# Performance work log

Hardware: AMD Instinct MI355X
Metric: run time of the kernel (lower is better)

Reference implementation:

```python
import jax, jax.numpy as jnp
import numpy as np

N_QUBITS = 10
Q_DEPTH = 6
MAX_LAYERS = 15
DIM = 2 ** N_QUBITS


def _apply_1q(s, U, w):
    # s: (B, 2^n) real statevector (circuit uses only H/RY/CNOT, all real).
    # Wire 0 is the most-significant bit (PennyLane convention).
    a, b = 2 ** w, 2 ** (N_QUBITS - 1 - w)
    s = s.reshape(-1, a, 2, b)
    if U.ndim == 2:  # gate shared across batch
        s = jnp.einsum('ij,Bajb->Baib', U, s)
    else:            # per-sample gate, U: (B,2,2)
        s = jnp.einsum('Bij,Bajb->Baib', U, s)
    return s.reshape(-1, DIM)


def _apply_cnot(s, c, t):
    # CNOT, control c < target t
    s = s.reshape(-1, 2 ** c, 2, 2 ** (t - c - 1), 2, 2 ** (N_QUBITS - 1 - t))
    s = jnp.stack([s[:, :, 0], jnp.flip(s[:, :, 1], axis=3)], axis=2)
    return s.reshape(-1, DIM)


def _ry(theta):
    # RY(theta) = [[cos t/2, -sin t/2], [sin t/2, cos t/2]]; theta scalar or (B,)
    c, si = jnp.cos(theta / 2.0), jnp.sin(theta / 2.0)
    return jnp.stack([jnp.stack([c, -si], -1), jnp.stack([si, c], -1)], -2)


def _quantum_net(q_in, q_params):
    # q_in: (B, n_qubits) rotation angles; q_params: (max_layers*n_qubits,)
    B = q_in.shape[0]
    qw = q_params.reshape(MAX_LAYERS, N_QUBITS)
    s = jnp.zeros((B, DIM), q_in.dtype).at[:, 0].set(1.0)  # |0...0>
    H = jnp.array([[1.0, 1.0], [1.0, -1.0]], q_in.dtype) / jnp.sqrt(jnp.asarray(2.0, q_in.dtype))
    for w in range(N_QUBITS):
        s = _apply_1q(s, H, w)
    for w in range(N_QUBITS):
        s = _apply_1q(s, _ry(q_in[:, w]), w)
    for k in range(Q_DEPTH):
        for i in range(0, N_QUBITS - 1, 2):
            s = _apply_cnot(s, i, i + 1)
        for i in range(1, N_QUBITS - 1, 2):
            s = _apply_cnot(s, i, i + 1)
        for w in range(N_QUBITS):
            s = _apply_1q(s, _ry(qw[k + 1, w]), w)
    probs = s * s
    # <Z_w> = P(bit_w = 0) - P(bit_w = 1)
    z = []
    for w in range(N_QUBITS):
        p = probs.reshape(-1, 2 ** w, 2, 2 ** (N_QUBITS - 1 - w)).sum(axis=(1, 3))
        z.append(p[:, 0] - p[:, 1])
    return jnp.stack(z, axis=1)  # (B, n_qubits)


def setup_inputs() -> dict:
    key = jax.random.key(0)
    ks = jax.random.split(key, 6)
    B, F, NQ, NC = 8192, 512, N_QUBITS, 2
    q_delta = 0.01
    return {
        'input_features': jax.random.normal(ks[0], (B, F), jnp.float32),
        'W_pre': jax.random.normal(ks[1], (NQ, F), jnp.float32) / np.sqrt(F),
        'b_pre': jnp.zeros((NQ,), jnp.float32),
        'q_params': q_delta * jax.random.normal(ks[2], (MAX_LAYERS * NQ,), jnp.float32),
        'W_post': jax.random.normal(ks[3], (NC, NQ), jnp.float32) / np.sqrt(NQ),
        'b_post': jnp.zeros((NC,), jnp.float32),
    }


def reference(input_features, W_pre, b_pre, q_params, W_post, b_post):
    pre_out = input_features @ W_pre.T + b_pre          # (B, n_qubits)
    q_in = jnp.tanh(pre_out) * (np.pi / 2.0)            # scale to [-pi/2, pi/2]
    q_out = _quantum_net(q_in, q_params)                # (B, n_qubits) PauliZ expvals
    return q_out @ W_post.T + b_post                    # (B, n_classes)
```

## Files before the change

### kernel.cpp

```cpp
#include <hip/hip_runtime.h>
#include <math.h>


#define NQ   10
#define NREG 16
#define DIM  1024

typedef _Float16 f16;
typedef _Float16 f16x8 __attribute__((ext_vector_type(8)));
typedef float    f32x4 __attribute__((ext_vector_type(4)));

template<int BB>
__device__ __forceinline__ void ry_lane(float (&s)[NREG], int lane, float c, float si) {
    float sgn = ((lane >> BB) & 1) ? si : -si;
    #pragma unroll
    for (int r = 0; r < NREG; ++r) {
        float o = __shfl_xor(s[r], 1 << BB);
        s[r] = fmaf(sgn, o, c * s[r]);
    }
}
template<int P>
__device__ __forceinline__ void ry_reg(float (&s)[NREG], float c, float si) {
    const int m = 1 << P;
    #pragma unroll
    for (int r = 0; r < NREG; ++r) {
        if ((r & m) == 0) {
            float a = s[r], b = s[r + m];
            s[r]     = fmaf(c, a, -si * b);
            s[r + m] = fmaf(si, a,  c * b);
        }
    }
}
__device__ __forceinline__ void cnot_5_6(float (&s)[NREG], int lane) {
    bool sel = (lane & 1) != 0;
    #pragma unroll
    for (int r = 0; r < 8; ++r) {
        float a = s[r], b = s[r + 8];
        s[r]     = sel ? b : a;
        s[r + 8] = sel ? a : b;
    }
}
template<int PC, int PT>
__device__ __forceinline__ void cnot_reg(float (&s)[NREG]) {
    #pragma unroll
    for (int r = 0; r < NREG; ++r) {
        if (((r >> PC) & 1) && !((r >> PT) & 1)) {
            float t = s[r];
            s[r] = s[r ^ (1 << PT)];
            s[r ^ (1 << PT)] = t;
        }
    }
}
__device__ __forceinline__ void perm_even(float (&s)[NREG], int lane) {
    int src = lane ^ (((((lane >> 5) & 1) << 4)) | ((((lane >> 3) & 1) << 2)) | (((lane >> 1) & 1)));
    #pragma unroll
    for (int r = 0; r < NREG; ++r) s[r] = __shfl(s[r], src);
}
__device__ __forceinline__ void perm_odd(float (&s)[NREG], int lane) {
    int src = lane ^ (((((lane >> 4) & 1) << 3)) | ((((lane >> 2) & 1) << 1)));
    #pragma unroll
    for (int r = 0; r < NREG; ++r) s[r] = __shfl(s[r], src);
}

#define APPLY_RY_ALL(CARR, SARR, BASE)                                        \
    { float c_, s_;                                                           \
      c_=__shfl(CARR,(BASE)+0); s_=__shfl(SARR,(BASE)+0); ry_lane<5>(s,lane,c_,s_); \
      c_=__shfl(CARR,(BASE)+1); s_=__shfl(SARR,(BASE)+1); ry_lane<4>(s,lane,c_,s_); \
      c_=__shfl(CARR,(BASE)+2); s_=__shfl(SARR,(BASE)+2); ry_lane<3>(s,lane,c_,s_); \
      c_=__shfl(CARR,(BASE)+3); s_=__shfl(SARR,(BASE)+3); ry_lane<2>(s,lane,c_,s_); \
      c_=__shfl(CARR,(BASE)+4); s_=__shfl(SARR,(BASE)+4); ry_lane<1>(s,lane,c_,s_); \
      c_=__shfl(CARR,(BASE)+5); s_=__shfl(SARR,(BASE)+5); ry_lane<0>(s,lane,c_,s_); \
      c_=__shfl(CARR,(BASE)+6); s_=__shfl(SARR,(BASE)+6); ry_reg<3>(s,c_,s_);       \
      c_=__shfl(CARR,(BASE)+7); s_=__shfl(SARR,(BASE)+7); ry_reg<2>(s,c_,s_);       \
      c_=__shfl(CARR,(BASE)+8); s_=__shfl(SARR,(BASE)+8); ry_reg<1>(s,c_,s_);       \
      c_=__shfl(CARR,(BASE)+9); s_=__shfl(SARR,(BASE)+9); ry_reg<0>(s,c_,s_); }

__device__ __forceinline__ void async16(const void* g, void* l) {
    __builtin_amdgcn_global_load_lds(
        (const __attribute__((address_space(1))) void*)g,
        (__attribute__((address_space(3))) void*)l, 16, 0, 0);
}

__global__ __launch_bounds__(256) void ka_prepare(
    const float* __restrict__ X, const float* __restrict__ Wpre,
    const float* __restrict__ bpre, const float* __restrict__ qp,
    f16* __restrict__ psi0, f16* __restrict__ Arm, float* __restrict__ z, int B)
{
    const int tid = threadIdx.x, lane = tid & 63, wv = tid >> 6;

    {
        int idx = blockIdx.x * 256 + tid;
        if (idx < 8192 * NQ) z[idx] = 0.0f;
    }

    for (int it = 0; it < 4; ++it) {
        int sample = blockIdx.x * 16 + wv * 4 + it;
        if (sample >= B) break;
        const float* xrow = X + (size_t)sample * 512;
        float4 x0 = ((const float4*)xrow)[lane];
        float4 x1 = ((const float4*)xrow)[64 + lane];
        float acc[NQ];
        #pragma unroll
        for (int q = 0; q < NQ; ++q) {
            const float* wr = Wpre + q * 512;
            float4 w0 = ((const float4*)wr)[lane];
            float4 w1 = ((const float4*)wr)[64 + lane];
            float a = x0.x * w0.x;
            a = fmaf(x0.y, w0.y, a); a = fmaf(x0.z, w0.z, a); a = fmaf(x0.w, w0.w, a);
            a = fmaf(x1.x, w1.x, a); a = fmaf(x1.y, w1.y, a);
            a = fmaf(x1.z, w1.z, a); a = fmaf(x1.w, w1.w, a);
            acc[q] = a;
        }
        #pragma unroll
        for (int q = 0; q < NQ; ++q) {
            float v = acc[q];
            #pragma unroll
            for (int d = 32; d >= 1; d >>= 1) v += __shfl_xor(v, d);
            acc[q] = v;
        }
        float pre = acc[0];
        #pragma unroll
        for (int q = 1; q < NQ; ++q) pre = (lane == q) ? acc[q] : pre;
        float c45 = 0.0f, s45 = 0.0f;
        if (lane < NQ) {
            float th = tanhf(pre + bpre[lane]) * 1.5707963267948966f;
            sincosf(0.5f * th + 0.7853981633974483f, &s45, &c45);
        }
        float lv = 1.0f;
        #pragma unroll
        for (int w = 0; w < 6; ++w) {
            float f0 = __shfl(c45, w), f1 = __shfl(s45, w);
            lv *= ((lane >> (5 - w)) & 1) ? f1 : f0;
        }
        float c6 = __shfl(c45, 6), s6 = __shfl(s45, 6);
        float c7 = __shfl(c45, 7), s7 = __shfl(s45, 7);
        float c8 = __shfl(c45, 8), s8 = __shfl(s45, 8);
        float c9 = __shfl(c45, 9), s9 = __shfl(s45, 9);
        float g01[4] = {c6 * c7, c6 * s7, s6 * c7, s6 * s7};
        float g23[4] = {c8 * c9, c8 * s9, s8 * c9, s8 * s9};
        union { f16 h[16]; float4 v[2]; } u;
        #pragma unroll
        for (int r = 0; r < NREG; ++r)
            u.h[r] = (f16)(lv * g01[r >> 2] * g23[r & 3]);
        float4* dst = (float4*)((char*)psi0 + (size_t)sample * 2048 + lane * 32);
        dst[0] = u.v[0];
        dst[1] = u.v[1];
    }

    if (wv < 2) {
        int row = blockIdx.x * 2 + wv;
        if (row < DIM) {
            float cw = 1.0f, swn = 0.0f;
            if (lane < 60) {
                float s_, c_;
                sincosf(0.5f * qp[10 + lane], &s_, &c_);
                cw = c_; swn = -s_;
            }
            float s[NREG];
            int srcLane = row >> 4, srcReg = row & 15;
            #pragma unroll
            for (int r = 0; r < NREG; ++r)
                s[r] = (lane == srcLane && r == srcReg) ? 1.0f : 0.0f;
            for (int kk = 6; kk >= 1; --kk) {
                APPLY_RY_ALL(cw, swn, (kk - 1) * 10);
                perm_odd(s, lane);
                cnot_5_6(s, lane);
                cnot_reg<2, 1>(s);
                perm_even(s, lane);
                cnot_reg<3, 2>(s);
                cnot_reg<1, 0>(s);
            }
            union { f16 h[16]; float4 v[2]; } u;
            #pragma unroll
            for (int r = 0; r < NREG; ++r) u.h[r] = (f16)s[r];
            float4* dst = (float4*)((char*)Arm + (size_t)row * 2048 + lane * 32);
            dst[0] = u.v[0];
            dst[1] = u.v[1];
        }
    }
}

__global__ __launch_bounds__(256, 4) void kb_gemm_measure(
    const f16* __restrict__ psi0, const f16* __restrict__ Arm,
    float* __restrict__ z)
{
    __shared__ __align__(16) char smem[24576];
    const int tid = threadIdx.x, lane = tid & 63, wv = tid >> 6;

    const int mB = blockIdx.x & 127, nB = blockIdx.x >> 7;
    const size_t tM = (size_t)mB * 64, tN = (size_t)nB * 128;
    f16* As = (f16*)smem;
    f16* Bs = (f16*)(smem + 8192);
    const int wm = (wv >> 1) * 32, wn = (wv & 1) * 64;

    f32x4 acc[2][4] = {};

    const f16* ga[2]; int ldsoA[2];
    #pragma unroll
    for (int p = 0; p < 2; ++p) {
        int slot = p * 256 + tid;
        int row = slot >> 3, gp = slot & 7, g = gp ^ (row & 7);
        ga[p] = psi0 + (tM + row) * 1024 + g * 8;
        ldsoA[p] = slot * 16;
    }
    const f16* gb[4]; int ldsoB[4];
    #pragma unroll
    for (int p = 0; p < 4; ++p) {
        int slot = p * 256 + tid;
        int row = slot >> 3, gp = slot & 7, g = gp ^ (row & 7);
        gb[p] = Arm + (tN + row) * 1024 + g * 8;
        ldsoB[p] = slot * 16;
    }

    for (int kt = 0; kt < 1024; kt += 64) {
        __syncthreads();
        #pragma unroll
        for (int p = 0; p < 2; ++p) async16(ga[p] + kt, (char*)As + ldsoA[p]);
        #pragma unroll
        for (int p = 0; p < 4; ++p) async16(gb[p] + kt, (char*)Bs + ldsoB[p]);
        __syncthreads();
        #pragma unroll
        for (int ks = 0; ks < 2; ++ks) {
            f16x8 af[2], bf[4];
            const int gpb = ks * 4 + (lane >> 4);
            const int gpx = gpb ^ (lane & 7);
            #pragma unroll
            for (int i = 0; i < 2; ++i) {
                int rowA = wm + i * 16 + (lane & 15);
                af[i] = *(const f16x8*)(As + rowA * 64 + gpx * 8);
            }
            #pragma unroll
            for (int j = 0; j < 4; ++j) {
                int rowB = wn + j * 16 + (lane & 15);
                bf[j] = *(const f16x8*)(Bs + rowB * 64 + gpx * 8);
            }
            #pragma unroll
            for (int i = 0; i < 2; ++i)
                #pragma unroll
                for (int j = 0; j < 4; ++j)
                    acc[i][j] = __builtin_amdgcn_mfma_f32_16x16x32_f16(af[i], bf[j], acc[i][j], 0, 0, 0);
        }
    }

    __syncthreads();
    float* zb = (float*)smem + (wn ? 640 : 0);
    const float sg0 = (nB & 4) ? -1.0f : 1.0f;
    const float sg1 = (nB & 2) ? -1.0f : 1.0f;
    const float sg2 = (nB & 1) ? -1.0f : 1.0f;
    const float sg3 = wn ? -1.0f : 1.0f;

    #pragma unroll
    for (int i = 0; i < 2; ++i) {
        #pragma unroll
        for (int t = 0; t < 4; ++t) {
            float p0 = acc[i][0][t] * acc[i][0][t];
            float p1 = acc[i][1][t] * acc[i][1][t];
            float p2 = acc[i][2][t] * acc[i][2][t];
            float p3 = acc[i][3][t] * acc[i][3][t];
            float t0  = (p0 + p1) + (p2 + p3);
            float tw5 = (p0 - p1) + (p2 - p3);
            float tw4 = (p0 + p1) - (p2 + p3);
            float s1 = __shfl_xor(t0, 1);
            float Av = t0 + s1;
            float Bv = (lane & 1) ? s1 - t0 : t0 - s1;
            float sA = __shfl_xor(Av, 2), sB = __shfl_xor(Bv, 2);
            float AP = Av + sA;
            float AM = (lane & 2) ? sA - Av : Av - sA;
            float BP = Bv + sB;
            float sAP = __shfl_xor(AP, 4), sAM = __shfl_xor(AM, 4), sBP = __shfl_xor(BP, 4);
            float APP = AP + sAP;
            float APM = (lane & 4) ? sAP - AP : AP - sAP;
            float AMP = AM + sAM;
            float BPP = BP + sBP;
            float a1 = __shfl_xor(APP, 8), a2 = __shfl_xor(APM, 8);
            float a3 = __shfl_xor(AMP, 8), a4 = __shfl_xor(BPP, 8);
            float T0 = APP + a1;
            float S6 = (lane & 8) ? a1 - APP : APP - a1;
            float S7 = APM + a2;
            float S8 = AMP + a3;
            float S9 = BPP + a4;
            float T5 = tw5, T4 = tw4;
            T5 += __shfl_xor(T5, 1); T5 += __shfl_xor(T5, 2);
            T5 += __shfl_xor(T5, 4); T5 += __shfl_xor(T5, 8);
            T4 += __shfl_xor(T4, 1); T4 += __shfl_xor(T4, 2);
            T4 += __shfl_xor(T4, 4); T4 += __shfl_xor(T4, 8);
            if ((lane & 15) == 0) {
                int row = wm + i * 16 + (lane >> 4) * 4 + t;
                float* d = zb + row * 10;
                d[0] = sg0 * T0; d[1] = sg1 * T0; d[2] = sg2 * T0; d[3] = sg3 * T0;
                d[4] = T4; d[5] = T5;
                d[6] = S6; d[7] = S7; d[8] = S8; d[9] = S9;
            }
        }
    }
    __syncthreads();
    float* zall = (float*)smem;
    for (int idx = tid; idx < 640; idx += 256) {
        float v = zall[idx] + zall[640 + idx];
        int row = idx / 10, w = idx - row * 10;
        atomicAdd(&z[((size_t)tM + row) * 10 + w], v);
    }
}

__global__ __launch_bounds__(256) void kc_post(
    const float* __restrict__ z, const float* __restrict__ Wpost,
    const float* __restrict__ bpost, float* __restrict__ out, int B)
{
    int gid = blockIdx.x * 256 + threadIdx.x;
    if (gid >= B) return;
    const float* zp = z + (size_t)gid * NQ;
    float o0 = bpost[0], o1 = bpost[1];
    #pragma unroll
    for (int w = 0; w < NQ; ++w) {
        float zw = zp[w];
        o0 = fmaf(zw, Wpost[w], o0);
        o1 = fmaf(zw, Wpost[NQ + w], o1);
    }
    out[(size_t)gid * 2 + 0] = o0;
    out[(size_t)gid * 2 + 1] = o1;
}

template<int BC, int BT>
__device__ __forceinline__ void cnot_lane(float (&s)[NREG], int lane) {
    int src = ((lane >> BC) & 1) ? (lane ^ (1 << BT)) : lane;
    #pragma unroll
    for (int r = 0; r < NREG; ++r) s[r] = __shfl(s[r], src);
}

__global__ __launch_bounds__(256) void hybrid_head_fallback(
    const float* __restrict__ X, const float* __restrict__ Wpre,
    const float* __restrict__ bpre, const float* __restrict__ qp,
    const float* __restrict__ Wpost, const float* __restrict__ bpost,
    float* __restrict__ out, int B)
{
    const int lane = threadIdx.x & 63;
    const int wave = threadIdx.x >> 6;
    const int sample = blockIdx.x * 4 + wave;
    if (sample >= B) return;

    const float* xrow = X + (size_t)sample * 512;
    float4 x0 = ((const float4*)xrow)[lane];
    float4 x1 = ((const float4*)xrow)[64 + lane];
    float acc[NQ];
    #pragma unroll
    for (int q = 0; q < NQ; ++q) {
        const float* wr = Wpre + q * 512;
        float4 w0 = ((const float4*)wr)[lane];
        float4 w1 = ((const float4*)wr)[64 + lane];
        float a = x0.x * w0.x;
        a = fmaf(x0.y, w0.y, a); a = fmaf(x0.z, w0.z, a); a = fmaf(x0.w, w0.w, a);
        a = fmaf(x1.x, w1.x, a); a = fmaf(x1.y, w1.y, a);
        a = fmaf(x1.z, w1.z, a); a = fmaf(x1.w, w1.w, a);
        acc[q] = a;
    }
    #pragma unroll
    for (int q = 0; q < NQ; ++q) {
        float v = acc[q];
        #pragma unroll
        for (int d = 32; d >= 1; d >>= 1) v += __shfl_xor(v, d);
        acc[q] = v;
    }
    float pre = acc[0];
    #pragma unroll
    for (int q = 1; q < NQ; ++q) pre = (lane == q) ? acc[q] : pre;
    float cth = 1.0f, sth = 0.0f;
    if (lane < NQ) {
        float th = tanhf(pre + bpre[lane]) * 1.5707963267948966f;
        sincosf(0.5f * th, &sth, &cth);
    }
    float cw = 1.0f, sw = 0.0f;
    if (lane < 60) sincosf(0.5f * qp[10 + lane], &sw, &cw);

    float s[NREG];
    #pragma unroll
    for (int r = 0; r < NREG; ++r) s[r] = 0.03125f;
    APPLY_RY_ALL(cth, sth, 0);
    for (int k = 0; k < 6; ++k) {
        perm_even(s, lane);
        cnot_reg<3, 2>(s);
        cnot_reg<1, 0>(s);
        perm_odd(s, lane);
        cnot_5_6(s, lane);
        cnot_reg<2, 1>(s);
        APPLY_RY_ALL(cw, sw, k * 10);
    }
    float p[NREG], tot = 0.0f;
    #pragma unroll
    for (int r = 0; r < NREG; ++r) { p[r] = s[r] * s[r]; tot += p[r]; }
    float z[NQ];
    #pragma unroll
    for (int w = 0; w < 6; ++w) z[w] = ((lane >> (5 - w)) & 1) ? -tot : tot;
    z[6] = z[7] = z[8] = z[9] = 0.0f;
    #pragma unroll
    for (int r = 0; r < NREG; ++r) {
        z[6] += ((r >> 3) & 1) ? -p[r] : p[r];
        z[7] += ((r >> 2) & 1) ? -p[r] : p[r];
        z[8] += ((r >> 1) & 1) ? -p[r] : p[r];
        z[9] += ((r >> 0) & 1) ? -p[r] : p[r];
    }
    #pragma unroll
    for (int w = 0; w < NQ; ++w) {
        float v = z[w];
        #pragma unroll
        for (int d = 32; d >= 1; d >>= 1) v += __shfl_xor(v, d);
        z[w] = v;
    }
    if (lane < 2) {
        const float* wp = Wpost + lane * NQ;
        float o = bpost[lane];
        #pragma unroll
        for (int w = 0; w < NQ; ++w) o = fmaf(z[w], wp[w], o);
        out[(size_t)sample * 2 + lane] = o;
    }
}

extern "C" void kernel_launch(void* const* d_in, const int* in_sizes, int n_in,
                              void* d_out, int out_size, void* d_ws, size_t ws_size,
                              hipStream_t stream) {
    const float* X     = (const float*)d_in[0];
    const float* Wpre  = (const float*)d_in[1];
    const float* bpre  = (const float*)d_in[2];
    const float* qp    = (const float*)d_in[3];
    const float* Wpost = (const float*)d_in[4];
    const float* bpost = (const float*)d_in[5];
    float* out = (float*)d_out;
    int B = in_sizes[0] / 512;

    size_t psi0_b = (size_t)B * DIM * sizeof(f16);
    size_t arm_b  = (size_t)DIM * DIM * sizeof(f16);
    size_t z_b    = (size_t)B * NQ * sizeof(float);
    size_t need = psi0_b + arm_b + z_b;

    if (B != 8192 || ws_size < need) {
        hipLaunchKernelGGL(hybrid_head_fallback, dim3((B + 3) / 4), dim3(256), 0, stream,
                           X, Wpre, bpre, qp, Wpost, bpost, out, B);
        return;
    }

    char* ws = (char*)d_ws;
    f16*   psi0 = (f16*)ws;
    f16*   Arm  = (f16*)(ws + psi0_b);
    float* z    = (float*)(ws + psi0_b + arm_b);

    hipLaunchKernelGGL(ka_prepare, dim3(512), dim3(256), 0, stream,
                       X, Wpre, bpre, qp, psi0, Arm, z, B);
    hipLaunchKernelGGL(kb_gemm_measure, dim3(1024), dim3(256), 0, stream,
                       psi0, Arm, z);
    hipLaunchKernelGGL(kc_post, dim3(32), dim3(256), 0, stream,
                       z, Wpost, bpost, out, B);
}
```

Before: 124.9 us.

## Fuse post-projection into GEMM via last-block counter and enlarge GEMM tiles

The GEMM kernel now loads MFMA fragments straight from global memory instead of staging them through LDS with async loads, and uses 128x128 tiles per block (512 blocks, 4x4 MFMA tiles per wave). The separate post-processing kernel is folded into the GEMM kernel: a per-row-tile atomic counter marks the last of the 8 column blocks, and that block computes the output projection. The prepare kernel now handles one sample per wave across 2048 blocks and also zeroes the counters. The aim is to save a launch and LDS traffic and to reuse each load more, at the cost of uncoalesced direct global fragment loads, higher register pressure and lower occupancy.

```diff
diff --git a/kernel.cpp b/kernel.cpp
--- a/kernel.cpp
+++ b/kernel.cpp
@@ -75,76 +75,73 @@
       c_=__shfl(CARR,(BASE)+8); s_=__shfl(SARR,(BASE)+8); ry_reg<1>(s,c_,s_);       \
       c_=__shfl(CARR,(BASE)+9); s_=__shfl(SARR,(BASE)+9); ry_reg<0>(s,c_,s_); }
 
-__device__ __forceinline__ void async16(const void* g, void* l) {
-    __builtin_amdgcn_global_load_lds(
-        (const __attribute__((address_space(1))) void*)g,
-        (__attribute__((address_space(3))) void*)l, 16, 0, 0);
-}
-
 __global__ __launch_bounds__(256) void ka_prepare(
     const float* __restrict__ X, const float* __restrict__ Wpre,
     const float* __restrict__ bpre, const float* __restrict__ qp,
-    f16* __restrict__ psi0, f16* __restrict__ Arm, float* __restrict__ z, int B)
+    f16* __restrict__ psi0, f16* __restrict__ Arm, float* __restrict__ z,
+    int* __restrict__ cnt, int B)
 {
     const int tid = threadIdx.x, lane = tid & 63, wv = tid >> 6;
 
     {
         int idx = blockIdx.x * 256 + tid;
         if (idx < 8192 * NQ) z[idx] = 0.0f;
-    }
-
-    for (int it = 0; it < 4; ++it) {
-        int sample = blockIdx.x * 16 + wv * 4 + it;
-        if (sample >= B) break;
-        const float* xrow = X + (size_t)sample * 512;
-        float4 x0 = ((const float4*)xrow)[lane];
-        float4 x1 = ((const float4*)xrow)[64 + lane];
-        float acc[NQ];
-        #pragma unroll
-        for (int q = 0; q < NQ; ++q) {
-            const float* wr = Wpre + q * 512;
-            float4 w0 = ((const float4*)wr)[lane];
-            float4 w1 = ((const float4*)wr)[64 + lane];
-            float a = x0.x * w0.x;
-            a = fmaf(x0.y, w0.y, a); a = fmaf(x0.z, w0.z, a); a = fmaf(x0.w, w0.w, a);
-            a = fmaf(x1.x, w1.x, a); a = fmaf(x1.y, w1.y, a);
-            a = fmaf(x1.z, w1.z, a); a = fmaf(x1.w, w1.w, a);
-            acc[q] = a;
-        }
-        #pragma unroll
-        for (int q = 0; q < NQ; ++q) {
-            float v = acc[q];
-            #pragma unroll
-            for (int d = 32; d >= 1; d >>= 1) v += __shfl_xor(v, d);
-            acc[q] = v;
-        }
-        float pre = acc[0];
-        #pragma unroll
-        for (int q = 1; q < NQ; ++q) pre = (lane == q) ? acc[q] : pre;
-        float c45 = 0.0f, s45 = 0.0f;
-        if (lane < NQ) {
-            float th = tanhf(pre + bpre[lane]) * 1.5707963267948966f;
-            sincosf(0.5f * th + 0.7853981633974483f, &s45, &c45);
-        }
-        float lv = 1.0f;
-        #pragma unroll
-        for (int w = 0; w < 6; ++w) {
-            float f0 = __shfl(c45, w), f1 = __shfl(s45, w);
-            lv *= ((lane >> (5 - w)) & 1) ? f1 : f0;
-        }
-        float c6 = __shfl(c45, 6), s6 = __shfl(s45, 6);
-        float c7 = __shfl(c45, 7), s7 = __shfl(s45, 7);
-        float c8 = __shfl(c45, 8), s8 = __shfl(s45, 8);
-        float c9 = __shfl(c45, 9), s9 = __shfl(s45, 9);
-        float g01[4] = {c6 * c7, c6 * s7, s6 * c7, s6 * s7};
-        float g23[4] = {c8 * c9, c8 * s9, s8 * c9, s8 * s9};
-        union { f16 h[16]; float4 v[2]; } u;
-        #pragma unroll
-        for (int r = 0; r < NREG; ++r)
-            u.h[r] = (f16)(lv * g01[r >> 2] * g23[r & 3]);
-        float4* dst = (float4*)((char*)psi0 + (size_t)sample * 2048 + lane * 32);
-        dst[0] = u.v[0];
-        dst[1] = u.v[1];
+        else if (idx < 8192 * NQ + 64) cnt[idx - 8192 * NQ] = 0;
+    }
+
+    {
+        int sample = blockIdx.x * 4 + wv;
+        if (sample < B) {
+            const float* xrow = X + (size_t)sample * 512;
+            float4 x0 = ((const float4*)xrow)[lane];
+            float4 x1 = ((const float4*)xrow)[64 + lane];
+            float acc[NQ];
+            #pragma unroll
+            for (int q = 0; q < NQ; ++q) {
+                const float* wr = Wpre + q * 512;
+                float4 w0 = ((const float4*)wr)[lane];
+                float4 w1 = ((const float4*)wr)[64 + lane];
+                float a = x0.x * w0.x;
+                a = fmaf(x0.y, w0.y, a); a = fmaf(x0.z, w0.z, a); a = fmaf(x0.w, w0.w, a);
+                a = fmaf(x1.x, w1.x, a); a = fmaf(x1.y, w1.y, a);
+                a = fmaf(x1.z, w1.z, a); a = fmaf(x1.w, w1.w, a);
+                acc[q] = a;
+            }
+            #pragma unroll
+            for (int q = 0; q < NQ; ++q) {
+                float v = acc[q];
+                #pragma unroll
+                for (int d = 32; d >= 1; d >>= 1) v += __shfl_xor(v, d);
+                acc[q] = v;
+            }
+            float pre = acc[0];
+            #pragma unroll
+            for (int q = 1; q < NQ; ++q) pre = (lane == q) ? acc[q] : pre;
+            float c45 = 0.0f, s45 = 0.0f;
+            if (lane < NQ) {
+                float th = tanhf(pre + bpre[lane]) * 1.5707963267948966f;
+                sincosf(0.5f * th + 0.7853981633974483f, &s45, &c45);
+            }
+            float lv = 1.0f;
+            #pragma unroll
+            for (int w = 0; w < 6; ++w) {
+                float f0 = __shfl(c45, w), f1 = __shfl(s45, w);
+                lv *= ((lane >> (5 - w)) & 1) ? f1 : f0;
+            }
+            float c6 = __shfl(c45, 6), s6 = __shfl(s45, 6);
+            float c7 = __shfl(c45, 7), s7 = __shfl(s45, 7);
+            float c8 = __shfl(c45, 8), s8 = __shfl(s45, 8);
+            float c9 = __shfl(c45, 9), s9 = __shfl(s45, 9);
+            float g01[4] = {c6 * c7, c6 * s7, s6 * c7, s6 * s7};
+            float g23[4] = {c8 * c9, c8 * s9, s8 * c9, s8 * s9};
+            union { f16 h[16]; float4 v[2]; } u;
+            #pragma unroll
+            for (int r = 0; r < NREG; ++r)
+                u.h[r] = (f16)(lv * g01[r >> 2] * g23[r & 3]);
+            float4* dst = (float4*)((char*)psi0 + (size_t)sample * 2048 + lane * 32);
+            dst[0] = u.v[0];
+            dst[1] = u.v[1];
+        }
     }
 
     if (wv < 2) {
@@ -180,77 +177,45 @@
     }
 }
 
-__global__ __launch_bounds__(256, 4) void kb_gemm_measure(
+__global__ __launch_bounds__(256, 3) void kb_gemm_measure(
     const f16* __restrict__ psi0, const f16* __restrict__ Arm,
-    float* __restrict__ z)
+    const float* __restrict__ Wpost, const float* __restrict__ bpost,
+    float* __restrict__ z, int* __restrict__ cnt, float* __restrict__ out)
 {
-    __shared__ __align__(16) char smem[24576];
+    __shared__ float zbuf[2560];
+    __shared__ int amLast;
     const int tid = threadIdx.x, lane = tid & 63, wv = tid >> 6;
-
-    const int mB = blockIdx.x & 127, nB = blockIdx.x >> 7;
-    const size_t tM = (size_t)mB * 64, tN = (size_t)nB * 128;
-    f16* As = (f16*)smem;
-    f16* Bs = (f16*)(smem + 8192);
-    const int wm = (wv >> 1) * 32, wn = (wv & 1) * 64;
-
-    f32x4 acc[2][4] = {};
-
-    const f16* ga[2]; int ldsoA[2];
-    #pragma unroll
-    for (int p = 0; p < 2; ++p) {
-        int slot = p * 256 + tid;
-        int row = slot >> 3, gp = slot & 7, g = gp ^ (row & 7);
-        ga[p] = psi0 + (tM + row) * 1024 + g * 8;
-        ldsoA[p] = slot * 16;
-    }
-    const f16* gb[4]; int ldsoB[4];
-    #pragma unroll
-    for (int p = 0; p < 4; ++p) {
-        int slot = p * 256 + tid;
-        int row = slot >> 3, gp = slot & 7, g = gp ^ (row & 7);
-        gb[p] = Arm + (tN + row) * 1024 + g * 8;
-        ldsoB[p] = slot * 16;
-    }
-
-    for (int kt = 0; kt < 1024; kt += 64) {
-        __syncthreads();
-        #pragma unroll
-        for (int p = 0; p < 2; ++p) async16(ga[p] + kt, (char*)As + ldsoA[p]);
-        #pragma unroll
-        for (int p = 0; p < 4; ++p) async16(gb[p] + kt, (char*)Bs + ldsoB[p]);
-        __syncthreads();
-        #pragma unroll
-        for (int ks = 0; ks < 2; ++ks) {
-            f16x8 af[2], bf[4];
-            const int gpb = ks * 4 + (lane >> 4);
-            const int gpx = gpb ^ (lane & 7);
-            #pragma unroll
-            for (int i = 0; i < 2; ++i) {
-                int rowA = wm + i * 16 + (lane & 15);
-                af[i] = *(const f16x8*)(As + rowA * 64 + gpx * 8);
-            }
-            #pragma unroll
-            for (int j = 0; j < 4; ++j) {
-                int rowB = wn + j * 16 + (lane & 15);
-                bf[j] = *(const f16x8*)(Bs + rowB * 64 + gpx * 8);
-            }
-            #pragma unroll
-            for (int i = 0; i < 2; ++i)
-                #pragma unroll
-                for (int j = 0; j < 4; ++j)
-                    acc[i][j] = __builtin_amdgcn_mfma_f32_16x16x32_f16(af[i], bf[j], acc[i][j], 0, 0, 0);
-        }
-    }
-
-    __syncthreads();
-    float* zb = (float*)smem + (wn ? 640 : 0);
+    const int mB = blockIdx.x & 63, nB = blockIdx.x >> 6;
+    const size_t tM = (size_t)mB * 128, tN = (size_t)nB * 128;
+    const int wm = (wv >> 1) * 64, wn = (wv & 1) * 64;
+
+    f32x4 acc[4][4] = {};
+
+    const f16* pa = psi0 + (tM + wm + (lane & 15)) * 1024 + (lane >> 4) * 8;
+    const f16* pb = Arm  + (tN + wn + (lane & 15)) * 1024 + (lane >> 4) * 8;
+
+    #pragma unroll 2
+    for (int kt = 0; kt < 1024; kt += 32) {
+        f16x8 af[4], bf[4];
+        #pragma unroll
+        for (int i = 0; i < 4; ++i) af[i] = *(const f16x8*)(pa + i * 16 * 1024 + kt);
+        #pragma unroll
+        for (int j = 0; j < 4; ++j) bf[j] = *(const f16x8*)(pb + j * 16 * 1024 + kt);
+        #pragma unroll
+        for (int i = 0; i < 4; ++i)
+            #pragma unroll
+            for (int j = 0; j < 4; ++j)
+                acc[i][j] = __builtin_amdgcn_mfma_f32_16x16x32_f16(af[i], bf[j], acc[i][j], 0, 0, 0);
+    }
+
+    float* zb = zbuf + (wn ? 1280 : 0);
     const float sg0 = (nB & 4) ? -1.0f : 1.0f;
     const float sg1 = (nB & 2) ? -1.0f : 1.0f;
     const float sg2 = (nB & 1) ? -1.0f : 1.0f;
     const float sg3 = wn ? -1.0f : 1.0f;
 
     #pragma unroll
-    for (int i = 0; i < 2; ++i) {
+    for (int i = 0; i < 4; ++i) {
         #pragma unroll
         for (int t = 0; t < 4; ++t) {
             float p0 = acc[i][0][t] * acc[i][0][t];
@@ -294,30 +259,30 @@
         }
     }
     __syncthreads();
-    float* zall = (float*)smem;
-    for (int idx = tid; idx < 640; idx += 256) {
-        float v = zall[idx] + zall[640 + idx];
+    for (int idx = tid; idx < 1280; idx += 256) {
+        float v = zbuf[idx] + zbuf[1280 + idx];
         int row = idx / 10, w = idx - row * 10;
         atomicAdd(&z[((size_t)tM + row) * 10 + w], v);
     }
-}
-
-__global__ __launch_bounds__(256) void kc_post(
-    const float* __restrict__ z, const float* __restrict__ Wpost,
-    const float* __restrict__ bpost, float* __restrict__ out, int B)
-{
-    int gid = blockIdx.x * 256 + threadIdx.x;
-    if (gid >= B) return;
-    const float* zp = z + (size_t)gid * NQ;
-    float o0 = bpost[0], o1 = bpost[1];
-    #pragma unroll
-    for (int w = 0; w < NQ; ++w) {
-        float zw = zp[w];
-        o0 = fmaf(zw, Wpost[w], o0);
-        o1 = fmaf(zw, Wpost[NQ + w], o1);
-    }
-    out[(size_t)gid * 2 + 0] = o0;
-    out[(size_t)gid * 2 + 1] = o1;
+
+    __threadfence();
+    __syncthreads();
+    if (tid == 0) amLast = (atomicAdd(&cnt[mB], 1) == 7);
+    __syncthreads();
+    if (amLast) {
+        for (int r = tid; r < 128; r += 256) {
+            float* zp = &z[((size_t)tM + r) * 10];
+            float o0 = bpost[0], o1 = bpost[1];
+            #pragma unroll
+            for (int w = 0; w < NQ; ++w) {
+                float zw = atomicAdd(&zp[w], 0.0f);
+                o0 = fmaf(zw, Wpost[w], o0);
+                o1 = fmaf(zw, Wpost[NQ + w], o1);
+            }
+            out[((size_t)tM + r) * 2 + 0] = o0;
+            out[((size_t)tM + r) * 2 + 1] = o1;
+        }
+    }
 }
 
 template<int BC, int BT>
@@ -429,7 +394,8 @@
     size_t psi0_b = (size_t)B * DIM * sizeof(f16);
     size_t arm_b  = (size_t)DIM * DIM * sizeof(f16);
     size_t z_b    = (size_t)B * NQ * sizeof(float);
-    size_t need = psi0_b + arm_b + z_b;
+    size_t cnt_b  = 64 * sizeof(int);
+    size_t need = psi0_b + arm_b + z_b + cnt_b;
 
     if (B != 8192 || ws_size < need) {
         hipLaunchKernelGGL(hybrid_head_fallback, dim3((B + 3) / 4), dim3(256), 0, stream,
@@ -441,11 +407,10 @@
     f16*   psi0 = (f16*)ws;
     f16*   Arm  = (f16*)(ws + psi0_b);
     float* z    = (float*)(ws + psi0_b + arm_b);
-
-    hipLaunchKernelGGL(ka_prepare, dim3(512), dim3(256), 0, stream,
-                       X, Wpre, bpre, qp, psi0, Arm, z, B);
-    hipLaunchKernelGGL(kb_gemm_measure, dim3(1024), dim3(256), 0, stream,
-                       psi0, Arm, z);
-    hipLaunchKernelGGL(kc_post, dim3(32), dim3(256), 0, stream,
-                       z, Wpost, bpost, out, B);
-}
+    int*   cnt  = (int*)(ws + psi0_b + arm_b + z_b);
+
+    hipLaunchKernelGGL(ka_prepare, dim3(2048), dim3(256), 0, stream,
+                       X, Wpre, bpre, qp, psi0, Arm, z, cnt, B);
+    hipLaunchKernelGGL(kb_gemm_measure, dim3(512), dim3(256), 0, stream,
+                       psi0, Arm, Wpost, bpost, z, cnt, out);
+}
```

After: 181.8 us. 1.46x slower.
